# Kernel tuning notes

Measured on AMD Instinct MI355X. Metric: run time of the kernel, lower is better.

## Reference

```python
import jax, jax.numpy as jnp
import numpy as np

# ---- module hyperparameters (from init_kwargs) ----
BOX = 256          # box_size
SIG = 1.5          # gaussian kernel sigma (pixels)
K = 9              # kernel_size = ceil(6*sig), made odd
HALF = K // 2
N = 50000          # n_points
LAT = 10           # latent_dim
NEUR = 32          # n_neurons
NLAYERS = 3        # n_layers
B = 16             # batch


def _uniform(key, shape, fan_in):
    a = 1.0 / np.sqrt(fan_in)
    return jax.random.uniform(key, shape, jnp.float32, -a, a)


def setup_inputs() -> dict:
    key = jax.random.key(0)
    ks = jax.random.split(key, 12)
    z = jax.random.normal(ks[0], (B, LAT), jnp.float32)
    # random proper rotation matrices via QR (faithful to cryo-EM poses)
    m = jax.random.normal(ks[1], (B, 3, 3), jnp.float32)
    q, _ = jnp.linalg.qr(m)
    r = q * jnp.sign(jnp.linalg.det(q))[:, None, None]
    ini = jnp.array([0.5, 0.5, 1.0], jnp.float32)
    pos_param = 0.1 * (jax.random.uniform(ks[2], (N, 3), jnp.float32) - ini)
    amp = 0.1 * jnp.ones((1,), jnp.float32)
    lin0_w = _uniform(ks[3], (NEUR, 3 + LAT - 1), 3 + LAT - 1)   # bias=False
    deform_w = _uniform(ks[4], (NLAYERS, NEUR, NEUR), NEUR)
    deform_b = _uniform(ks[5], (NLAYERS, NEUR), NEUR)
    lin1a_w = _uniform(ks[6], (3, NEUR), NEUR)                    # bias=False
    lin1b_w = _uniform(ks[7], (3, 3), 3)                          # bias=False
    linamp_w = _uniform(ks[8], (N, 1), 1)
    linamp_b = _uniform(ks[9], (N,), 1)
    return {"z": z, "r": r, "pos_param": pos_param, "amp": amp,
            "lin0_w": lin0_w, "deform_w": deform_w, "deform_b": deform_b,
            "lin1a_w": lin1a_w, "lin1b_w": lin1b_w,
            "linamp_w": linamp_w, "linamp_b": linamp_b, "d": 1}


def _splat(proj, amps):
    """Gaussian splat of points onto a BOXxBOX grid.
    proj: (B, N, 2) in [-0.5, 0.5];  amps: (B, N).  Returns (B, BOX, BOX)."""
    px = (proj + 0.5) * (BOX - 1)                  # pixel coords (B,N,2)
    c = jnp.floor(px + 0.5)                        # nearest pixel center
    off = jnp.arange(K, dtype=px.dtype) - HALF     # (K,)
    g0 = c[..., 0:1] + off                         # (B,N,K) grid coords dim0
    g1 = c[..., 1:2] + off                         # (B,N,K) grid coords dim1
    inv2s2 = 1.0 / (2.0 * SIG * SIG)
    w0 = jnp.exp(-(g0 - px[..., 0:1]) ** 2 * inv2s2)
    w1 = jnp.exp(-(g1 - px[..., 1:2]) ** 2 * inv2s2)
    w0 = w0 * ((g0 >= 0) & (g0 <= BOX - 1))       # mask out-of-bounds taps
    w1 = w1 * ((g1 >= 0) & (g1 <= BOX - 1))
    vals = amps[..., None, None] * w0[..., :, None] * w1[..., None, :]  # (B,N,K,K)
    i0 = jnp.clip(g0, 0, BOX - 1).astype(jnp.int32)
    i1 = jnp.clip(g1, 0, BOX - 1).astype(jnp.int32)

    def scat(i0b, i1b, vb):                        # per image scatter-add
        iy = jnp.broadcast_to(i0b[:, :, None], vb.shape).reshape(-1)
        ix = jnp.broadcast_to(i1b[:, None, :], vb.shape).reshape(-1)
        return jnp.zeros((BOX, BOX), vb.dtype).at[iy, ix].add(vb.reshape(-1))

    return jax.vmap(scat)(i0, i1, vals)


def _forward(z, r, pos_param, amp, lin0_w, deform_w, deform_b,
             lin1a_w, lin1b_w, linamp_w, linamp_b, d):
    bsz = z.shape[0]
    posi = jnp.broadcast_to(pos_param, (bsz, N, 3))
    if d > 0:
        conf = jnp.broadcast_to(z[:, None, :-1], (bsz, N, LAT - 1))
        h = jnp.concatenate([posi, conf], axis=-1) @ lin0_w.T   # (B,N,NEUR)
        for l in range(NLAYERS):                                # residual relu blocks
            h = jax.nn.relu(h @ deform_w[l].T + deform_b[l]) + h
        res = jnp.tanh(h @ lin1a_w.T) @ lin1b_w.T               # (B,N,3)
        pos = posi + res
    else:
        res = jnp.zeros_like(posi)
        pos = posi
    amp_corr = jax.nn.sigmoid(z[:, -1:] @ linamp_w.T + linamp_b)  # (B,N)
    proj_pos = jnp.einsum('bnj,bjk->bnk', pos, r)[..., :2]        # rotate + project
    amps = amp_corr * amp[0]
    img = _splat(proj_pos, amps)
    return img, img, proj_pos, pos, res


def reference(z, r, pos_param, amp, lin0_w, deform_w, deform_b,
              lin1a_w, lin1b_w, linamp_w, linamp_b, d):
    return _forward(z, r, pos_param, amp, lin0_w, deform_w, deform_b,
                    lin1a_w, lin1b_w, linamp_w, linamp_b, d)
```

## Files before the change

kernel.cpp:

```cpp
#include <hip/hip_runtime.h>
#include <math.h>

#define BOX   256
#define NPTS  50000
#define LATD  10
#define NEUR  32
#define NLAY  3
#define BATCH 16

#define MTPB  256
#define MBLKX ((NPTS + MTPB - 1)/MTPB)

#define PTPB  256
#define PBLKX ((NPTS + PTPB - 1)/PTPB)

#define CELLS_X 64
#define CELLS   (CELLS_X*CELLS_X)
#define PREF_STRIDE 4104
#define CHUNK   128
#define WCAP    4608

#define GBLK    128

#define IMG_ELEMS (BATCH*BOX*BOX)
#define OFF_IMG2  (IMG_ELEMS)
#define OFF_PROJ  (2*IMG_ELEMS)
#define OFF_POS   (OFF_PROJ + BATCH*NPTS*2)
#define OFF_RES   (OFF_POS  + BATCH*NPTS*3)

#define WS_COUNTS 0
#define WS_NWORK  (BATCH*CELLS)
#define WS_PREFIX (WS_NWORK + BATCH)
#define WS_WORK   (WS_PREFIX + BATCH*PREF_STRIDE)
#define WS_AUX    (WS_WORK + BATCH*WCAP)
#define WS_INTS   (WS_AUX + BATCH*NPTS)

#define HSTRH 40

typedef _Float16 f16x8 __attribute__((ext_vector_type(8)));
typedef _Float16 f16x4 __attribute__((ext_vector_type(4)));
typedef float    f32x4 __attribute__((ext_vector_type(4)));

#if __has_builtin(__builtin_amdgcn_exp2f)
#define EXP2R(x) __builtin_amdgcn_exp2f(x)
#else
#define EXP2R(x) exp2f(x)
#endif

__device__ __forceinline__ float fast_tanh(float x) {
    return 1.0f - 2.0f / (__expf(2.0f * x) + 1.0f);
}

__global__ __launch_bounds__(MTPB) void mlp_bin(
    const float* __restrict__ z, const float* __restrict__ r,
    const float* __restrict__ pos_param, const float* __restrict__ amp,
    const float* __restrict__ lin0_w, const float* __restrict__ deform_w,
    const float* __restrict__ deform_b, const float* __restrict__ lin1a_w,
    const float* __restrict__ lin1b_w, const float* __restrict__ linamp_w,
    const float* __restrict__ linamp_b, const int* __restrict__ dflag,
    float* __restrict__ out, int* __restrict__ counts, int* __restrict__ aux)
{
    __shared__ __align__(16) unsigned char s_raw[4*64*HSTRH*2 + NEUR*4];
    _Float16* s_h   = (_Float16*)s_raw;
    float*    s_z   = (float*)(s_raw + 4*64*HSTRH*2);
    int*      s_cnt = (int*)s_raw;

    const int b     = blockIdx.y;
    const int tid   = threadIdx.x;
    const int wave  = tid >> 6;
    const int lane  = tid & 63;
    const int cfrag = lane & 15;
    const int rq    = lane >> 4;
    const int k0    = rq * 8;
    _Float16* __restrict__ s_hw = s_h + wave*64*HSTRH;

    if (tid < NEUR) {
        float acc = 0.f;
        #pragma unroll
        for (int j = 0; j < LATD-1; j++)
            acc = fmaf(lin0_w[tid*12 + 3 + j], z[b*LATD + j], acc);
        s_z[tid] = acc;
    }
    __syncthreads();

    const int n  = blockIdx.x*MTPB + tid;
    const bool v0 = (n < NPTS);
    const int m0 = v0 ? n : (NPTS-1);
    const int dd = *dflag;

    const float p0w = pos_param[m0*3+0], p1w = pos_param[m0*3+1], p2w = pos_param[m0*3+2];

    float res0 = 0.f, res1 = 0.f, res2 = 0.f;

    if (dd > 0) {
        f16x8 bfrag[NLAY][2];
        float bias_c[NLAY][2];
        #pragma unroll
        for (int l = 0; l < NLAY; ++l) {
            #pragma unroll
            for (int nt = 0; nt < 2; ++nt) {
                const int c = cfrag + 16*nt;
                const float* wp = deform_w + l*NEUR*NEUR + c*NEUR + k0;
                const f32x4 w0 = *(const f32x4*)wp;
                const f32x4 w1 = *(const f32x4*)(wp + 4);
                f16x8 bv;
                bv[0]=(_Float16)w0[0]; bv[1]=(_Float16)w0[1];
                bv[2]=(_Float16)w0[2]; bv[3]=(_Float16)w0[3];
                bv[4]=(_Float16)w1[0]; bv[5]=(_Float16)w1[1];
                bv[6]=(_Float16)w1[2]; bv[7]=(_Float16)w1[3];
                bfrag[l][nt]  = bv;
                bias_c[l][nt] = deform_b[l*NEUR + c];
            }
        }

        #pragma unroll
        for (int o4 = 0; o4 < 8; ++o4) {
            f16x4 h4;
            #pragma unroll
            for (int jj = 0; jj < 4; ++jj) {
                const int o = o4*4 + jj;
                h4[jj] = (_Float16)fmaf(lin0_w[o*12+0], p0w,
                                   fmaf(lin0_w[o*12+1], p1w,
                                   fmaf(lin0_w[o*12+2], p2w, s_z[o])));
            }
            *(f16x4*)&s_hw[lane*HSTRH + o4*4] = h4;
        }
        __syncthreads();

        float rs0[4][4], rs1[4][4];
        #pragma unroll
        for (int mt = 0; mt < 4; ++mt) {
            #pragma unroll
            for (int rr = 0; rr < 4; ++rr) {
                const int row = 16*mt + 4*rq + rr;
                rs0[mt][rr] = (float)s_hw[row*HSTRH + cfrag];
                rs1[mt][rr] = (float)s_hw[row*HSTRH + cfrag + 16];
            }
        }

        const f32x4 zc = {0.f, 0.f, 0.f, 0.f};
        #pragma unroll
        for (int l = 0; l < NLAY; ++l) {
            f16x8 af[4];
            #pragma unroll
            for (int mt = 0; mt < 4; ++mt)
                af[mt] = *(const f16x8*)&s_hw[(16*mt + cfrag)*HSTRH + k0];
            f32x4 ac0[4], ac1[4];
            #pragma unroll
            for (int mt = 0; mt < 4; ++mt) {
                ac0[mt] = __builtin_amdgcn_mfma_f32_16x16x32_f16(af[mt], bfrag[l][0], zc, 0, 0, 0);
                ac1[mt] = __builtin_amdgcn_mfma_f32_16x16x32_f16(af[mt], bfrag[l][1], zc, 0, 0, 0);
            }
            __syncthreads();
            const float b0l = bias_c[l][0], b1l = bias_c[l][1];
            #pragma unroll
            for (int mt = 0; mt < 4; ++mt) {
                #pragma unroll
                for (int rr = 0; rr < 4; ++rr) {
                    const int row = 16*mt + 4*rq + rr;
                    const float h0n = fmaxf(ac0[mt][rr] + b0l, 0.f) + rs0[mt][rr];
                    const float h1n = fmaxf(ac1[mt][rr] + b1l, 0.f) + rs1[mt][rr];
                    rs0[mt][rr] = h0n;
                    rs1[mt][rr] = h1n;
                    s_hw[row*HSTRH + cfrag]      = (_Float16)h0n;
                    s_hw[row*HSTRH + cfrag + 16] = (_Float16)h1n;
                }
            }
            __syncthreads();
        }

        float t0 = 0.f, t1 = 0.f, t2 = 0.f;
        #pragma unroll
        for (int ch = 0; ch < 4; ++ch) {
            const f16x8 hv = *(const f16x8*)&s_hw[lane*HSTRH + ch*8];
            #pragma unroll
            for (int jj = 0; jj < 8; ++jj) {
                const int j = ch*8 + jj;
                const float hf = (float)hv[jj];
                t0 = fmaf(lin1a_w[0*NEUR + j], hf, t0);
                t1 = fmaf(lin1a_w[1*NEUR + j], hf, t1);
                t2 = fmaf(lin1a_w[2*NEUR + j], hf, t2);
            }
        }
        t0 = fast_tanh(t0); t1 = fast_tanh(t1); t2 = fast_tanh(t2);
        res0 = fmaf(t0, lin1b_w[0], fmaf(t1, lin1b_w[1], t2*lin1b_w[2]));
        res1 = fmaf(t0, lin1b_w[3], fmaf(t1, lin1b_w[4], t2*lin1b_w[5]));
        res2 = fmaf(t0, lin1b_w[6], fmaf(t1, lin1b_w[7], t2*lin1b_w[8]));
    }

    const float r00 = r[b*9+0], r01 = r[b*9+1];
    const float r10 = r[b*9+3], r11 = r[b*9+4];
    const float r20 = r[b*9+6], r21 = r[b*9+7];

    int cell = 0;
    if (v0) {
        const float pos0 = p0w + res0, pos1 = p1w + res1, pos2 = p2w + res2;
        const float pj0 = fmaf(pos0, r00, fmaf(pos1, r10, pos2*r20));
        const float pj1 = fmaf(pos0, r01, fmaf(pos1, r11, pos2*r21));
        const long long bn = (long long)b*NPTS + n;
        out[OFF_PROJ + bn*2 + 0] = pj0;  out[OFF_PROJ + bn*2 + 1] = pj1;
        out[OFF_POS  + bn*3 + 0] = pos0; out[OFF_POS  + bn*3 + 1] = pos1;
        out[OFF_POS  + bn*3 + 2] = pos2;
        out[OFF_RES  + bn*3 + 0] = res0; out[OFF_RES + bn*3 + 1] = res1;
        out[OFF_RES  + bn*3 + 2] = res2;
        const float px0 = (pj0 + 0.5f) * (float)(BOX-1);
        const float px1 = (pj1 + 0.5f) * (float)(BOX-1);
        const int c0 = (int)fminf(fmaxf(floorf(px0 + 0.5f), 0.f), 255.f);
        const int c1 = (int)fminf(fmaxf(floorf(px1 + 0.5f), 0.f), 255.f);
        cell = (c0>>2)*CELLS_X + (c1>>2);
    }

    __syncthreads();
    for (int i = tid; i < CELLS; i += MTPB) s_cnt[i] = 0;
    __syncthreads();
    int rank = 0;
    if (v0) rank = atomicAdd(&s_cnt[cell], 1);
    __syncthreads();
    for (int c = tid; c < CELLS; c += MTPB) {
        const int cnt = s_cnt[c];
        if (cnt > 0) s_cnt[c] = atomicAdd(&counts[b*CELLS + c], cnt);
    }
    __syncthreads();
    if (v0) aux[b*NPTS + n] = (cell << 16) | (s_cnt[cell] + rank);
}

__global__ __launch_bounds__(1024) void scan_cells(
    const int* __restrict__ counts, int* __restrict__ prefix,
    int* __restrict__ n_work, int* __restrict__ work)
{
    __shared__ int wsum[16];
    __shared__ int s_nw;
    const int img = blockIdx.x, t = threadIdx.x;
    const int lane = t & 63, wid = t >> 6;
    if (t == 0) s_nw = 0;
    const int4 v = ((const int4*)(counts + img*CELLS))[t];
    const int s3 = v.x + v.y + v.z + v.w;

    int sc = s3;
    #pragma unroll
    for (int off = 1; off < 64; off <<= 1) {
        const int u = __shfl_up(sc, off, 64);
        if (lane >= off) sc += u;
    }
    if (lane == 63) wsum[wid] = sc;
    __syncthreads();
    if (wid == 0) {
        int ws = (lane < 16) ? wsum[lane] : 0;
        #pragma unroll
        for (int off = 1; off < 16; off <<= 1) {
            const int u = __shfl_up(ws, off, 64);
            if (lane >= off) ws += u;
        }
        if (lane < 16) wsum[lane] = ws;
    }
    __syncthreads();
    const int woff = (wid > 0) ? wsum[wid-1] : 0;
    const int incl = sc + woff;
    const int base = incl - s3;
    ((int4*)(prefix + img*PREF_STRIDE))[t] =
        make_int4(base, base+v.x, base+v.x+v.y, base+v.x+v.y+v.z);
    if (t == 1023) prefix[img*PREF_STRIDE + CELLS] = incl;

    const int cnts[4] = { v.x, v.y, v.z, v.w };
    #pragma unroll
    for (int i = 0; i < 4; i++) {
        const int cnt = cnts[i];
        if (cnt > 0) {
            const int c = 4*t + i;
            const int nch = (cnt + CHUNK - 1)/CHUNK;
            const int wb = atomicAdd(&s_nw, nch);
            for (int k = 0; k < nch; k++) work[img*WCAP + wb + k] = (c << 9) | k;
        }
    }
    __syncthreads();
    if (t == 0) n_work[img] = s_nw;
}

__global__ __launch_bounds__(PTPB) void place(
    const float* __restrict__ z, const float* __restrict__ amp,
    const float* __restrict__ linamp_w, const float* __restrict__ linamp_b,
    const float* __restrict__ out, const int* __restrict__ prefix,
    const int* __restrict__ aux, float4* __restrict__ recs, int* __restrict__ cursors)
{
    const int b = blockIdx.y;
    if (blockIdx.x == 0 && threadIdx.x == 0) cursors[b*64] = 0;
    const int n = blockIdx.x*PTPB + threadIdx.x;
    if (n >= NPTS) return;

    const long long bn = (long long)b*NPTS + n;
    const float pj0 = out[OFF_PROJ + bn*2 + 0];
    const float pj1 = out[OFF_PROJ + bn*2 + 1];
    const float lo = fmaf(z[b*LATD + LATD-1], linamp_w[n], linamp_b[n]);
    const float a  = amp[0] / (1.0f + __expf(-lo));
    const float px0 = (pj0 + 0.5f) * (float)(BOX-1);
    const float px1 = (pj1 + 0.5f) * (float)(BOX-1);

    const int av  = aux[b*NPTS + n];
    const int cell = av >> 16, wr = av & 0xFFFF;
    const int dst  = prefix[b*PREF_STRIDE + cell] + wr;
    recs[(long long)b*NPTS + dst] = make_float4(px0, px1, a, floorf(px0 + 0.5f));
}

__global__ __launch_bounds__(256) void gather_work(
    const float4* __restrict__ recs, const int* __restrict__ prefix,
    const int* __restrict__ n_work, const int* __restrict__ work,
    float* __restrict__ out, int* __restrict__ cursors)
{
    const int b    = blockIdx.y;
    const int lane = threadIdx.x & 63;
    const int nw   = n_work[b];
    int* __restrict__ cur = cursors + b*64;

    const int* __restrict__ P = prefix + b*PREF_STRIDE;
    const float4* __restrict__ R = recs + (long long)b*NPTS;
    float* __restrict__ img = out + (size_t)b*BOX*BOX;
    const float Kc  = -0.32059884f;
    const float K8  = 8.0f  * Kc;
    const float K16 = 16.0f * Kc;
    const float C32 = 0.00081582472f;

    for (;;) {
        int grab;
        if (lane == 0) grab = atomicAdd(cur, 1);
        const int it = __shfl(grab, 0, 64);
        if (it >= nw) break;

        const int wd   = __builtin_amdgcn_readfirstlane(work[b*WCAP + it]);
        const int cell = wd >> 9, kch = wd & 511;
        const int s = P[cell] + kch*CHUNK;
        const int e = min(P[cell+1], s + CHUNK);

        const int cy = cell >> 6, cx = cell & 63;
        const int col = lane & 15, r0 = lane >> 4;
        const int gx  = 4*cx - 4 + col;
        const int gy0 = 4*cy - 4 + r0;
        const float xf  = (float)gx;
        const float y0f = (float)gy0;
        const float frc = (float)(r0 + 4*cy);

        float a0 = 0.f, a1 = 0.f, a2 = 0.f;
        #pragma unroll 8
        for (int rr = s; rr < e; ++rr) {
            const float4 rc = R[rr];
            const float ry = rc.x, rx = rc.y, ra = rc.z, stf = rc.w;

            const float dx = xf - rx;
            const float dy = y0f - ry;
            const float d2 = fmaf(dy, dy, dx*dx);
            float g = ra * EXP2R(d2 * Kc);
            g = (fabsf(dx) <= 4.5f) ? g : 0.f;

            const float u  = EXP2R(fminf(fmaf(dy, K8, K16), 60.f));
            const float uu = (u * u) * C32;
            const float g0m = (frc >= stf) ? g  : 0.f;
            const float u2m = (frc <= stf) ? uu : 0.f;
            a0 += g0m;
            a1 = fmaf(g, u,   a1);
            a2 = fmaf(g, u2m, a2);
        }

        if (gx >= 0 && gx < BOX) {
            if (a0 != 0.f && gy0 >= 0)      atomicAdd(&img[ gy0     *BOX + gx], a0);
            if (a1 != 0.f)                  atomicAdd(&img[(gy0 + 4)*BOX + gx], a1);
            if (a2 != 0.f && gy0 + 8 < BOX) atomicAdd(&img[(gy0 + 8)*BOX + gx], a2);
        }
    }
}

__global__ __launch_bounds__(256) void copy_img(const float4* __restrict__ src,
                                                float4* __restrict__ dst, int n4)
{
    int i = blockIdx.x*blockDim.x + threadIdx.x;
    if (i < n4) dst[i] = src[i];
}

extern "C" void kernel_launch(void* const* d_in, const int* in_sizes, int n_in,
                              void* d_out, int out_size, void* d_ws, size_t ws_size,
                              hipStream_t stream)
{
    const float* z        = (const float*)d_in[0];
    const float* r        = (const float*)d_in[1];
    const float* posp     = (const float*)d_in[2];
    const float* amp      = (const float*)d_in[3];
    const float* lin0_w   = (const float*)d_in[4];
    const float* deform_w = (const float*)d_in[5];
    const float* deform_b = (const float*)d_in[6];
    const float* lin1a_w  = (const float*)d_in[7];
    const float* lin1b_w  = (const float*)d_in[8];
    const float* linamp_w = (const float*)d_in[9];
    const float* linamp_b = (const float*)d_in[10];
    const int*   dflag    = (const int*)d_in[11];
    float* out = (float*)d_out;

    int* ws_i    = (int*)d_ws;
    int* counts  = ws_i + WS_COUNTS;
    int* n_work  = ws_i + WS_NWORK;
    int* prefix  = ws_i + WS_PREFIX;
    int* work    = ws_i + WS_WORK;
    int* aux     = ws_i + WS_AUX;
    float4* recs = (float4*)((char*)d_ws + (size_t)WS_INTS*sizeof(int));

    hipMemsetAsync(counts, 0, (size_t)(BATCH*CELLS + BATCH)*sizeof(int), stream);
    hipMemsetAsync(out, 0, (size_t)IMG_ELEMS*sizeof(float), stream);

    dim3 gridM(MBLKX, BATCH);
    mlp_bin<<<gridM, MTPB, 0, stream>>>(z, r, posp, amp, lin0_w, deform_w, deform_b,
                                        lin1a_w, lin1b_w, linamp_w, linamp_b, dflag,
                                        out, counts, aux);

    scan_cells<<<BATCH, 1024, 0, stream>>>(counts, prefix, n_work, work);

    dim3 gridP(PBLKX, BATCH);
    place<<<gridP, PTPB, 0, stream>>>(z, amp, linamp_w, linamp_b, out, prefix, aux,
                                      recs, counts);

    dim3 gridG(GBLK, BATCH);
    gather_work<<<gridG, 256, 0, stream>>>(recs, prefix, n_work, work, out, counts);

    const int n4 = IMG_ELEMS/4;
    copy_img<<<(n4 + 255)/256, 256, 0, stream>>>((const float4*)out,
                                                 (float4*)(out + OFF_IMG2), n4);
}
```

Before: 193.7 us.

## Flatten gather grid with cross-batch work stealing and fuse image zeroing

The gather kernel switches from a per-batch 2D grid of 128 blocks each to a flat grid of 2048 blocks. Each wave walks every batch image in a staggered order and pulls work items from per-batch atomic cursors, prefetching the next grab while it computes. This is meant to balance uneven per-batch work and keep waves busy instead of leaving them idle once their own batch runs out. The separate memset of the output image is folded into the start of mlp_bin, removing one launch, at the cost of extra stores from that kernel.

```diff
diff --git a/kernel.cpp b/kernel.cpp
--- a/kernel.cpp
+++ b/kernel.cpp
@@ -20,7 +20,7 @@
 #define CHUNK   128
 #define WCAP    4608
 
-#define GBLK    128
+#define GBLKX   2048
 
 #define IMG_ELEMS (BATCH*BOX*BOX)
 #define OFF_IMG2  (IMG_ELEMS)
@@ -60,6 +60,12 @@
     const float* __restrict__ linamp_b, const int* __restrict__ dflag,
     float* __restrict__ out, int* __restrict__ counts, int* __restrict__ aux)
 {
+    {
+        const int gid = (blockIdx.y*gridDim.x + blockIdx.x)*MTPB + threadIdx.x;
+        if (gid < IMG_ELEMS/4)
+            ((float4*)out)[gid] = make_float4(0.f, 0.f, 0.f, 0.f);
+    }
+
     __shared__ __align__(16) unsigned char s_raw[4*64*HSTRH*2 + NEUR*4];
     _Float16* s_h   = (_Float16*)s_raw;
     float*    s_z   = (float*)(s_raw + 4*64*HSTRH*2);
@@ -306,63 +312,73 @@
     const int* __restrict__ n_work, const int* __restrict__ work,
     float* __restrict__ out, int* __restrict__ cursors)
 {
-    const int b    = blockIdx.y;
     const int lane = threadIdx.x & 63;
-    const int nw   = n_work[b];
-    int* __restrict__ cur = cursors + b*64;
-
-    const int* __restrict__ P = prefix + b*PREF_STRIDE;
-    const float4* __restrict__ R = recs + (long long)b*NPTS;
-    float* __restrict__ img = out + (size_t)b*BOX*BOX;
+    const int widx = blockIdx.x*4 + (threadIdx.x >> 6);
     const float Kc  = -0.32059884f;
     const float K8  = 8.0f  * Kc;
     const float K16 = 16.0f * Kc;
     const float C32 = 0.00081582472f;
 
-    for (;;) {
-        int grab;
-        if (lane == 0) grab = atomicAdd(cur, 1);
-        const int it = __shfl(grab, 0, 64);
-        if (it >= nw) break;
-
-        const int wd   = __builtin_amdgcn_readfirstlane(work[b*WCAP + it]);
-        const int cell = wd >> 9, kch = wd & 511;
-        const int s = P[cell] + kch*CHUNK;
-        const int e = min(P[cell+1], s + CHUNK);
-
-        const int cy = cell >> 6, cx = cell & 63;
-        const int col = lane & 15, r0 = lane >> 4;
-        const int gx  = 4*cx - 4 + col;
-        const int gy0 = 4*cy - 4 + r0;
-        const float xf  = (float)gx;
-        const float y0f = (float)gy0;
-        const float frc = (float)(r0 + 4*cy);
-
-        float a0 = 0.f, a1 = 0.f, a2 = 0.f;
-        #pragma unroll 8
-        for (int rr = s; rr < e; ++rr) {
-            const float4 rc = R[rr];
-            const float ry = rc.x, rx = rc.y, ra = rc.z, stf = rc.w;
-
-            const float dx = xf - rx;
-            const float dy = y0f - ry;
-            const float d2 = fmaf(dy, dy, dx*dx);
-            float g = ra * EXP2R(d2 * Kc);
-            g = (fabsf(dx) <= 4.5f) ? g : 0.f;
-
-            const float u  = EXP2R(fminf(fmaf(dy, K8, K16), 60.f));
-            const float uu = (u * u) * C32;
-            const float g0m = (frc >= stf) ? g  : 0.f;
-            const float u2m = (frc <= stf) ? uu : 0.f;
-            a0 += g0m;
-            a1 = fmaf(g, u,   a1);
-            a2 = fmaf(g, u2m, a2);
-        }
-
-        if (gx >= 0 && gx < BOX) {
-            if (a0 != 0.f && gy0 >= 0)      atomicAdd(&img[ gy0     *BOX + gx], a0);
-            if (a1 != 0.f)                  atomicAdd(&img[(gy0 + 4)*BOX + gx], a1);
-            if (a2 != 0.f && gy0 + 8 < BOX) atomicAdd(&img[(gy0 + 8)*BOX + gx], a2);
+    #pragma unroll 1
+    for (int pass = 0; pass < BATCH; ++pass) {
+        const int b  = (widx + pass) & (BATCH-1);
+        const int nw = n_work[b];
+        int* __restrict__ cur = cursors + b*64;
+        const int* __restrict__ P = prefix + b*PREF_STRIDE;
+        const float4* __restrict__ R = recs + (long long)b*NPTS;
+        const int* __restrict__ W = work + b*WCAP;
+        float* __restrict__ img = out + (size_t)b*BOX*BOX;
+
+        int nxt = 0;
+        if (lane == 0) nxt = atomicAdd(cur, 1);
+        nxt = __shfl(nxt, 0, 64);
+
+        while (nxt < nw) {
+            const int it = nxt;
+            int grab = 0;
+            if (lane == 0) grab = atomicAdd(cur, 1);
+
+            const int wd   = __builtin_amdgcn_readfirstlane(W[it]);
+            const int cell = wd >> 9, kch = wd & 511;
+            const int s = P[cell] + kch*CHUNK;
+            const int e = min(P[cell+1], s + CHUNK);
+
+            const int cy = cell >> 6, cx = cell & 63;
+            const int col = lane & 15, r0 = lane >> 4;
+            const int gx  = 4*cx - 4 + col;
+            const int gy0 = 4*cy - 4 + r0;
+            const float xf  = (float)gx;
+            const float y0f = (float)gy0;
+            const float frc = (float)(r0 + 4*cy);
+
+            float a0 = 0.f, a1 = 0.f, a2 = 0.f;
+            #pragma unroll 8
+            for (int rr = s; rr < e; ++rr) {
+                const float4 rc = R[rr];
+                const float ry = rc.x, rx = rc.y, ra = rc.z, stf = rc.w;
+
+                const float dx = xf - rx;
+                const float dy = y0f - ry;
+                const float d2 = fmaf(dy, dy, dx*dx);
+                float g = ra * EXP2R(d2 * Kc);
+                g = (fabsf(dx) <= 4.5f) ? g : 0.f;
+
+                const float u  = EXP2R(fminf(fmaf(dy, K8, K16), 60.f));
+                const float uu = (u * u) * C32;
+                const float g0m = (frc >= stf) ? g  : 0.f;
+                const float u2m = (frc <= stf) ? uu : 0.f;
+                a0 += g0m;
+                a1 = fmaf(g, u,   a1);
+                a2 = fmaf(g, u2m, a2);
+            }
+
+            if (gx >= 0 && gx < BOX) {
+                if (a0 != 0.f && gy0 >= 0)      atomicAdd(&img[ gy0     *BOX + gx], a0);
+                if (a1 != 0.f)                  atomicAdd(&img[(gy0 + 4)*BOX + gx], a1);
+                if (a2 != 0.f && gy0 + 8 < BOX) atomicAdd(&img[(gy0 + 8)*BOX + gx], a2);
+            }
+
+            nxt = __shfl(grab, 0, 64);
         }
     }
 }
@@ -401,7 +417,6 @@
     float4* recs = (float4*)((char*)d_ws + (size_t)WS_INTS*sizeof(int));
 
     hipMemsetAsync(counts, 0, (size_t)(BATCH*CELLS + BATCH)*sizeof(int), stream);
-    hipMemsetAsync(out, 0, (size_t)IMG_ELEMS*sizeof(float), stream);
 
     dim3 gridM(MBLKX, BATCH);
     mlp_bin<<<gridM, MTPB, 0, stream>>>(z, r, posp, amp, lin0_w, deform_w, deform_b,
@@ -414,8 +429,7 @@
     place<<<gridP, PTPB, 0, stream>>>(z, amp, linamp_w, linamp_b, out, prefix, aux,
                                       recs, counts);
 
-    dim3 gridG(GBLK, BATCH);
-    gather_work<<<gridG, 256, 0, stream>>>(recs, prefix, n_work, work, out, counts);
+    gather_work<<<dim3(GBLKX), 256, 0, stream>>>(recs, prefix, n_work, work, out, counts);
 
     const int n4 = IMG_ELEMS/4;
     copy_img<<<(n4 + 255)/256, 256, 0, stream>>>((const float4*)out,
```

New measurement: 254.8 us. 31.5% more time.

## Split scatter into index and fill passes, fold image zeroing, static work split

Applied to the files above, without the earlier changes.

Zeroing of the output image moves into the MLP kernel, replacing the separate memset. The point scatter is split into two passes: one writes each point's source index to its sorted slot, and a second fills the records in sorted order, so the large record writes become coalesced and the gathers read from the source instead. The gather kernel drops its atomic work-stealing cursor in favour of a static strided wave assignment, with twice as many blocks. This adds one extra kernel launch and risks load imbalance across waves, since chunk costs vary.

```diff
diff --git a/kernel.cpp b/kernel.cpp
--- a/kernel.cpp
+++ b/kernel.cpp
@@ -20,7 +20,8 @@
 #define CHUNK   128
 #define WCAP    4608
 
-#define GBLK    128
+#define GBLK    256
+#define GSTRIDE (GBLK*4)
 
 #define IMG_ELEMS (BATCH*BOX*BOX)
 #define OFF_IMG2  (IMG_ELEMS)
@@ -60,6 +61,12 @@
     const float* __restrict__ linamp_b, const int* __restrict__ dflag,
     float* __restrict__ out, int* __restrict__ counts, int* __restrict__ aux)
 {
+    {
+        const int gid = (blockIdx.y*gridDim.x + blockIdx.x)*MTPB + threadIdx.x;
+        if (gid < IMG_ELEMS/4)
+            ((float4*)out)[gid] = make_float4(0.f, 0.f, 0.f, 0.f);
+    }
+
     __shared__ __align__(16) unsigned char s_raw[4*64*HSTRH*2 + NEUR*4];
     _Float16* s_h   = (_Float16*)s_raw;
     float*    s_z   = (float*)(s_raw + 4*64*HSTRH*2);
@@ -276,16 +283,30 @@
     if (t == 0) n_work[img] = s_nw;
 }
 
-__global__ __launch_bounds__(PTPB) void place(
+__global__ __launch_bounds__(PTPB) void place_idx(
+    const int* __restrict__ aux, const int* __restrict__ prefix,
+    int* __restrict__ recs_i)
+{
+    const int b = blockIdx.y;
+    const int n = blockIdx.x*PTPB + threadIdx.x;
+    if (n >= NPTS) return;
+    const int av  = aux[b*NPTS + n];
+    const int cell = av >> 16, wr = av & 0xFFFF;
+    const int dst  = prefix[b*PREF_STRIDE + cell] + wr;
+    recs_i[((long long)b*NPTS + dst)*4 + 3] = n;
+}
+
+__global__ __launch_bounds__(PTPB) void place_fill(
     const float* __restrict__ z, const float* __restrict__ amp,
     const float* __restrict__ linamp_w, const float* __restrict__ linamp_b,
-    const float* __restrict__ out, const int* __restrict__ prefix,
-    const int* __restrict__ aux, float4* __restrict__ recs, int* __restrict__ cursors)
+    const float* __restrict__ out, float4* __restrict__ recs)
 {
     const int b = blockIdx.y;
-    if (blockIdx.x == 0 && threadIdx.x == 0) cursors[b*64] = 0;
-    const int n = blockIdx.x*PTPB + threadIdx.x;
-    if (n >= NPTS) return;
+    const int t = blockIdx.x*PTPB + threadIdx.x;
+    if (t >= NPTS) return;
+
+    const long long bt = (long long)b*NPTS + t;
+    const int n = ((const int*)recs)[bt*4 + 3];
 
     const long long bn = (long long)b*NPTS + n;
     const float pj0 = out[OFF_PROJ + bn*2 + 0];
@@ -294,22 +315,18 @@
     const float a  = amp[0] / (1.0f + __expf(-lo));
     const float px0 = (pj0 + 0.5f) * (float)(BOX-1);
     const float px1 = (pj1 + 0.5f) * (float)(BOX-1);
-
-    const int av  = aux[b*NPTS + n];
-    const int cell = av >> 16, wr = av & 0xFFFF;
-    const int dst  = prefix[b*PREF_STRIDE + cell] + wr;
-    recs[(long long)b*NPTS + dst] = make_float4(px0, px1, a, floorf(px0 + 0.5f));
+    recs[bt] = make_float4(px0, px1, a, floorf(px0 + 0.5f));
 }
 
 __global__ __launch_bounds__(256) void gather_work(
     const float4* __restrict__ recs, const int* __restrict__ prefix,
     const int* __restrict__ n_work, const int* __restrict__ work,
-    float* __restrict__ out, int* __restrict__ cursors)
+    float* __restrict__ out)
 {
     const int b    = blockIdx.y;
+    const int wave = blockIdx.x*4 + (threadIdx.x >> 6);
     const int lane = threadIdx.x & 63;
     const int nw   = n_work[b];
-    int* __restrict__ cur = cursors + b*64;
 
     const int* __restrict__ P = prefix + b*PREF_STRIDE;
     const float4* __restrict__ R = recs + (long long)b*NPTS;
@@ -319,12 +336,7 @@
     const float K16 = 16.0f * Kc;
     const float C32 = 0.00081582472f;
 
-    for (;;) {
-        int grab;
-        if (lane == 0) grab = atomicAdd(cur, 1);
-        const int it = __shfl(grab, 0, 64);
-        if (it >= nw) break;
-
+    for (int it = wave; it < nw; it += GSTRIDE) {
         const int wd   = __builtin_amdgcn_readfirstlane(work[b*WCAP + it]);
         const int cell = wd >> 9, kch = wd & 511;
         const int s = P[cell] + kch*CHUNK;
@@ -401,7 +413,6 @@
     float4* recs = (float4*)((char*)d_ws + (size_t)WS_INTS*sizeof(int));
 
     hipMemsetAsync(counts, 0, (size_t)(BATCH*CELLS + BATCH)*sizeof(int), stream);
-    hipMemsetAsync(out, 0, (size_t)IMG_ELEMS*sizeof(float), stream);
 
     dim3 gridM(MBLKX, BATCH);
     mlp_bin<<<gridM, MTPB, 0, stream>>>(z, r, posp, amp, lin0_w, deform_w, deform_b,
@@ -411,11 +422,11 @@
     scan_cells<<<BATCH, 1024, 0, stream>>>(counts, prefix, n_work, work);
 
     dim3 gridP(PBLKX, BATCH);
-    place<<<gridP, PTPB, 0, stream>>>(z, amp, linamp_w, linamp_b, out, prefix, aux,
-                                      recs, counts);
+    place_idx<<<gridP, PTPB, 0, stream>>>(aux, prefix, (int*)recs);
+    place_fill<<<gridP, PTPB, 0, stream>>>(z, amp, linamp_w, linamp_b, out, recs);
 
     dim3 gridG(GBLK, BATCH);
-    gather_work<<<gridG, 256, 0, stream>>>(recs, prefix, n_work, work, out, counts);
+    gather_work<<<gridG, 256, 0, stream>>>(recs, prefix, n_work, work, out);
 
     const int n4 = IMG_ELEMS/4;
     copy_img<<<(n4 + 255)/256, 256, 0, stream>>>((const float4*)out,
```

Result: slower. 199.3 us (+2.9%).

## Replace atomic work queue with global static work split and drop image copy kernel

Applied to the files above, without the earlier changes.

The gather kernel no longer pulls work items from a per-image atomic cursor. It computes a prefix over all images' work counts and walks a flat global work index with a grid stride across 2048 blocks, which spreads load across images. The separate copy kernel is removed: every atomic add is issued to both output images, doubling the output atomics and the memset size. The scan kernel is reshaped to 256 threads with 16 cells per thread, and the MLP grid is flattened to 1D. This saves a launch and the cursor atomics, at the cost of more global atomics and uncoalesced per-thread prefix stores.

```diff
diff --git a/kernel.cpp b/kernel.cpp
--- a/kernel.cpp
+++ b/kernel.cpp
@@ -10,6 +10,7 @@
 
 #define MTPB  256
 #define MBLKX ((NPTS + MTPB - 1)/MTPB)
+#define NTILES (MBLKX*BATCH)
 
 #define PTPB  256
 #define PBLKX ((NPTS + PTPB - 1)/PTPB)
@@ -20,7 +21,7 @@
 #define CHUNK   128
 #define WCAP    4608
 
-#define GBLK    128
+#define GBLKX   2048
 
 #define IMG_ELEMS (BATCH*BOX*BOX)
 #define OFF_IMG2  (IMG_ELEMS)
@@ -36,6 +37,7 @@
 #define WS_INTS   (WS_AUX + BATCH*NPTS)
 
 #define HSTRH 40
+#define LDS_BYTES (4*64*HSTRH*2 + NEUR*4)
 
 typedef _Float16 f16x8 __attribute__((ext_vector_type(8)));
 typedef _Float16 f16x4 __attribute__((ext_vector_type(4)));
@@ -51,21 +53,20 @@
     return 1.0f - 2.0f / (__expf(2.0f * x) + 1.0f);
 }
 
-__global__ __launch_bounds__(MTPB) void mlp_bin(
+__global__ __launch_bounds__(MTPB) void k_mlp(
     const float* __restrict__ z, const float* __restrict__ r,
-    const float* __restrict__ pos_param, const float* __restrict__ amp,
-    const float* __restrict__ lin0_w, const float* __restrict__ deform_w,
-    const float* __restrict__ deform_b, const float* __restrict__ lin1a_w,
-    const float* __restrict__ lin1b_w, const float* __restrict__ linamp_w,
-    const float* __restrict__ linamp_b, const int* __restrict__ dflag,
+    const float* __restrict__ pos_param, const float* __restrict__ lin0_w,
+    const float* __restrict__ deform_w, const float* __restrict__ deform_b,
+    const float* __restrict__ lin1a_w, const float* __restrict__ lin1b_w,
+    const int* __restrict__ dflag,
     float* __restrict__ out, int* __restrict__ counts, int* __restrict__ aux)
 {
-    __shared__ __align__(16) unsigned char s_raw[4*64*HSTRH*2 + NEUR*4];
+    __shared__ __align__(16) unsigned char s_raw[LDS_BYTES];
     _Float16* s_h   = (_Float16*)s_raw;
     float*    s_z   = (float*)(s_raw + 4*64*HSTRH*2);
     int*      s_cnt = (int*)s_raw;
 
-    const int b     = blockIdx.y;
+    const int tile  = blockIdx.x;
     const int tid   = threadIdx.x;
     const int wave  = tid >> 6;
     const int lane  = tid & 63;
@@ -74,6 +75,10 @@
     const int k0    = rq * 8;
     _Float16* __restrict__ s_hw = s_h + wave*64*HSTRH;
 
+    const int b  = tile / MBLKX;
+    const int tx = tile - b*MBLKX;
+    const int dd = *dflag;
+
     if (tid < NEUR) {
         float acc = 0.f;
         #pragma unroll
@@ -83,13 +88,11 @@
     }
     __syncthreads();
 
-    const int n  = blockIdx.x*MTPB + tid;
+    const int n  = tx*MTPB + tid;
     const bool v0 = (n < NPTS);
     const int m0 = v0 ? n : (NPTS-1);
-    const int dd = *dflag;
 
     const float p0w = pos_param[m0*3+0], p1w = pos_param[m0*3+1], p2w = pos_param[m0*3+2];
-
     float res0 = 0.f, res1 = 0.f, res2 = 0.f;
 
     if (dd > 0) {
@@ -224,66 +227,66 @@
     if (v0) aux[b*NPTS + n] = (cell << 16) | (s_cnt[cell] + rank);
 }
 
-__global__ __launch_bounds__(1024) void scan_cells(
+__global__ __launch_bounds__(MTPB) void k_scan(
     const int* __restrict__ counts, int* __restrict__ prefix,
     int* __restrict__ n_work, int* __restrict__ work)
 {
-    __shared__ int wsum[16];
-    __shared__ int s_nw;
-    const int img = blockIdx.x, t = threadIdx.x;
-    const int lane = t & 63, wid = t >> 6;
-    if (t == 0) s_nw = 0;
-    const int4 v = ((const int4*)(counts + img*CELLS))[t];
-    const int s3 = v.x + v.y + v.z + v.w;
-
-    int sc = s3;
+    __shared__ int swsum[4];
+    __shared__ int snw;
+    const int img = blockIdx.x, tid = threadIdx.x;
+    const int lane = tid & 63, wid = tid >> 6;
+    if (tid == 0) snw = 0;
+
+    int c[16];
+    const int4* cp = (const int4*)(counts + img*CELLS) + tid*4;
+    #pragma unroll
+    for (int q = 0; q < 4; ++q) {
+        const int4 v = cp[q];
+        c[q*4+0]=v.x; c[q*4+1]=v.y; c[q*4+2]=v.z; c[q*4+3]=v.w;
+    }
+    int pres[16]; int run = 0;
+    #pragma unroll
+    for (int i = 0; i < 16; ++i) { pres[i] = run; run += c[i]; }
+
+    int sc = run;
     #pragma unroll
     for (int off = 1; off < 64; off <<= 1) {
         const int u = __shfl_up(sc, off, 64);
         if (lane >= off) sc += u;
     }
-    if (lane == 63) wsum[wid] = sc;
-    __syncthreads();
-    if (wid == 0) {
-        int ws = (lane < 16) ? wsum[lane] : 0;
-        #pragma unroll
-        for (int off = 1; off < 16; off <<= 1) {
-            const int u = __shfl_up(ws, off, 64);
-            if (lane >= off) ws += u;
-        }
-        if (lane < 16) wsum[lane] = ws;
-    }
-    __syncthreads();
-    const int woff = (wid > 0) ? wsum[wid-1] : 0;
-    const int incl = sc + woff;
-    const int base = incl - s3;
-    ((int4*)(prefix + img*PREF_STRIDE))[t] =
-        make_int4(base, base+v.x, base+v.x+v.y, base+v.x+v.y+v.z);
-    if (t == 1023) prefix[img*PREF_STRIDE + CELLS] = incl;
-
-    const int cnts[4] = { v.x, v.y, v.z, v.w };
-    #pragma unroll
-    for (int i = 0; i < 4; i++) {
-        const int cnt = cnts[i];
+    if (lane == 63) swsum[wid] = sc;
+    __syncthreads();
+    int woff = 0;
+    #pragma unroll
+    for (int w = 0; w < 3; ++w) if (w < wid) woff += swsum[w];
+    const int base = woff + sc - run;
+
+    int* gpre = prefix + img*PREF_STRIDE;
+    #pragma unroll
+    for (int i = 0; i < 16; ++i) gpre[tid*16 + i] = base + pres[i];
+    if (tid == 255) gpre[CELLS] = woff + sc;
+
+    #pragma unroll
+    for (int i = 0; i < 16; ++i) {
+        const int cnt = c[i];
         if (cnt > 0) {
-            const int c = 4*t + i;
-            const int nch = (cnt + CHUNK - 1)/CHUNK;
-            const int wb = atomicAdd(&s_nw, nch);
-            for (int k = 0; k < nch; k++) work[img*WCAP + wb + k] = (c << 9) | k;
-        }
-    }
-    __syncthreads();
-    if (t == 0) n_work[img] = s_nw;
-}
-
-__global__ __launch_bounds__(PTPB) void place(
+            const int cell = tid*16 + i;
+            const int nch = (cnt + CHUNK - 1) >> 7;
+            const int wb = atomicAdd(&snw, nch);
+            for (int k = 0; k < nch; ++k) work[img*WCAP + wb + k] = (cell << 9) | k;
+        }
+    }
+    __syncthreads();
+    if (tid == 0) n_work[img] = snw;
+}
+
+__global__ __launch_bounds__(PTPB) void k_place(
     const float* __restrict__ z, const float* __restrict__ amp,
     const float* __restrict__ linamp_w, const float* __restrict__ linamp_b,
     const float* __restrict__ out, const int* __restrict__ prefix,
-    const int* __restrict__ aux, float4* __restrict__ recs, int* __restrict__ cursors)
+    const int* __restrict__ aux, float4* __restrict__ recs)
 {
     const int b = blockIdx.y;
-    if (blockIdx.x == 0 && threadIdx.x == 0) cursors[b*64] = 0;
     const int n = blockIdx.x*PTPB + threadIdx.x;
     if (n >= NPTS) return;
 
@@ -301,29 +304,39 @@
     recs[(long long)b*NPTS + dst] = make_float4(px0, px1, a, floorf(px0 + 0.5f));
 }
 
-__global__ __launch_bounds__(256) void gather_work(
+__global__ __launch_bounds__(MTPB) void k_gather(
     const float4* __restrict__ recs, const int* __restrict__ prefix,
     const int* __restrict__ n_work, const int* __restrict__ work,
-    float* __restrict__ out, int* __restrict__ cursors)
+    float* __restrict__ out)
 {
-    const int b    = blockIdx.y;
     const int lane = threadIdx.x & 63;
-    const int nw   = n_work[b];
-    int* __restrict__ cur = cursors + b*64;
-
-    const int* __restrict__ P = prefix + b*PREF_STRIDE;
-    const float4* __restrict__ R = recs + (long long)b*NPTS;
-    float* __restrict__ img = out + (size_t)b*BOX*BOX;
+    const int gw = blockIdx.x*4 + (threadIdx.x >> 6);
+    const int GW = gridDim.x*4;
     const float Kc  = -0.32059884f;
     const float K8  = 8.0f  * Kc;
     const float K16 = 16.0f * Kc;
     const float C32 = 0.00081582472f;
 
-    for (;;) {
-        int grab;
-        if (lane == 0) grab = atomicAdd(cur, 1);
-        const int it = __shfl(grab, 0, 64);
-        if (it >= nw) break;
+    int nwoff[BATCH+1];
+    nwoff[0] = 0;
+    #pragma unroll
+    for (int q = 0; q < BATCH; ++q) nwoff[q+1] = nwoff[q] + n_work[q];
+    const int total = nwoff[BATCH];
+
+    for (int g = gw; g < total; g += GW) {
+        int b = 0, base = 0;
+        #pragma unroll
+        for (int q = 0; q < BATCH; ++q) {
+            const bool geq = (g >= nwoff[q+1]);
+            b    = geq ? q+1        : b;
+            base = geq ? nwoff[q+1] : base;
+        }
+        const int it = g - base;
+
+        const int* __restrict__ P = prefix + b*PREF_STRIDE;
+        const float4* __restrict__ R = recs + (long long)b*NPTS;
+        float* __restrict__ img  = out + (size_t)b*BOX*BOX;
+        float* __restrict__ img2 = out + OFF_IMG2 + (size_t)b*BOX*BOX;
 
         const int wd   = __builtin_amdgcn_readfirstlane(work[b*WCAP + it]);
         const int cell = wd >> 9, kch = wd & 511;
@@ -343,35 +356,35 @@
         for (int rr = s; rr < e; ++rr) {
             const float4 rc = R[rr];
             const float ry = rc.x, rx = rc.y, ra = rc.z, stf = rc.w;
-
             const float dx = xf - rx;
             const float dy = y0f - ry;
             const float d2 = fmaf(dy, dy, dx*dx);
-            float g = ra * EXP2R(d2 * Kc);
-            g = (fabsf(dx) <= 4.5f) ? g : 0.f;
-
+            float gv = ra * EXP2R(d2 * Kc);
+            gv = (fabsf(dx) <= 4.5f) ? gv : 0.f;
             const float u  = EXP2R(fminf(fmaf(dy, K8, K16), 60.f));
             const float uu = (u * u) * C32;
-            const float g0m = (frc >= stf) ? g  : 0.f;
+            const float g0m = (frc >= stf) ? gv : 0.f;
             const float u2m = (frc <= stf) ? uu : 0.f;
             a0 += g0m;
-            a1 = fmaf(g, u,   a1);
-            a2 = fmaf(g, u2m, a2);
+            a1 = fmaf(gv, u,   a1);
+            a2 = fmaf(gv, u2m, a2);
         }
 
         if (gx >= 0 && gx < BOX) {
-            if (a0 != 0.f && gy0 >= 0)      atomicAdd(&img[ gy0     *BOX + gx], a0);
-            if (a1 != 0.f)                  atomicAdd(&img[(gy0 + 4)*BOX + gx], a1);
-            if (a2 != 0.f && gy0 + 8 < BOX) atomicAdd(&img[(gy0 + 8)*BOX + gx], a2);
-        }
-    }
-}
-
-__global__ __launch_bounds__(256) void copy_img(const float4* __restrict__ src,
-                                                float4* __restrict__ dst, int n4)
-{
-    int i = blockIdx.x*blockDim.x + threadIdx.x;
-    if (i < n4) dst[i] = src[i];
+            if (a0 != 0.f && gy0 >= 0) {
+                atomicAdd(&img [ gy0     *BOX + gx], a0);
+                atomicAdd(&img2[ gy0     *BOX + gx], a0);
+            }
+            if (a1 != 0.f) {
+                atomicAdd(&img [(gy0 + 4)*BOX + gx], a1);
+                atomicAdd(&img2[(gy0 + 4)*BOX + gx], a1);
+            }
+            if (a2 != 0.f && gy0 + 8 < BOX) {
+                atomicAdd(&img [(gy0 + 8)*BOX + gx], a2);
+                atomicAdd(&img2[(gy0 + 8)*BOX + gx], a2);
+            }
+        }
+    }
 }
 
 extern "C" void kernel_launch(void* const* d_in, const int* in_sizes, int n_in,
@@ -400,24 +413,16 @@
     int* aux     = ws_i + WS_AUX;
     float4* recs = (float4*)((char*)d_ws + (size_t)WS_INTS*sizeof(int));
 
-    hipMemsetAsync(counts, 0, (size_t)(BATCH*CELLS + BATCH)*sizeof(int), stream);
-    hipMemsetAsync(out, 0, (size_t)IMG_ELEMS*sizeof(float), stream);
-
-    dim3 gridM(MBLKX, BATCH);
-    mlp_bin<<<gridM, MTPB, 0, stream>>>(z, r, posp, amp, lin0_w, deform_w, deform_b,
-                                        lin1a_w, lin1b_w, linamp_w, linamp_b, dflag,
-                                        out, counts, aux);
-
-    scan_cells<<<BATCH, 1024, 0, stream>>>(counts, prefix, n_work, work);
+    hipMemsetAsync(counts, 0, (size_t)BATCH*CELLS*sizeof(int), stream);
+    hipMemsetAsync(out, 0, (size_t)2*IMG_ELEMS*sizeof(float), stream);
+
+    k_mlp<<<dim3(NTILES), MTPB, 0, stream>>>(z, r, posp, lin0_w, deform_w, deform_b,
+                                             lin1a_w, lin1b_w, dflag, out, counts, aux);
+
+    k_scan<<<dim3(BATCH), MTPB, 0, stream>>>(counts, prefix, n_work, work);
 
     dim3 gridP(PBLKX, BATCH);
-    place<<<gridP, PTPB, 0, stream>>>(z, amp, linamp_w, linamp_b, out, prefix, aux,
-                                      recs, counts);
-
-    dim3 gridG(GBLK, BATCH);
-    gather_work<<<gridG, 256, 0, stream>>>(recs, prefix, n_work, work, out, counts);
-
-    const int n4 = IMG_ELEMS/4;
-    copy_img<<<(n4 + 255)/256, 256, 0, stream>>>((const float4*)out,
-                                                 (float4*)(out + OFF_IMG2), n4);
-}
+    k_place<<<gridP, PTPB, 0, stream>>>(z, amp, linamp_w, linamp_b, out, prefix, aux, recs);
+
+    k_gather<<<dim3(GBLKX), MTPB, 0, stream>>>(recs, prefix, n_work, work, out);
+}
```

Measured after the change: 186.9 us. -3.5%, faster.
